# Kernel tuning notes

Hardware: AMD Instinct MI355X
Metric: run time of the kernel (lower is better)

The kernel has to match this reference:

```python
import jax, jax.numpy as jnp
import numpy as np

KH, KW, PAD = 32, 32, 10  # kernel_size and padding from NeuralMem.__init__


def setup_inputs() -> dict:
    key = jax.random.key(0)
    k1, k2, k3, k4 = jax.random.split(key, 4)
    image = jax.random.normal(k1, (64, 64, 3), dtype=jnp.float32)
    mem = jax.random.normal(k2, (8192, 3072), dtype=jnp.float32)    # faiss IndexFlatL2 bank (keys)
    mem2 = jax.random.normal(k3, (8192, 3072), dtype=jnp.float32)   # faiss reconstruction bank (values)
    mapping = jax.random.randint(k4, (8192,), 0, 8192)              # Counter.most_common(1) vote table
    return {"image": image, "mem": mem, "mem2": mem2, "mapping": mapping}


def reference(image, mem, mem2, mapping):
    H, W, C = image.shape
    x = image.transpose(2, 0, 1)                       # [C,H,W]  (permute(2,0,1))
    xp = jnp.pad(x, ((0, 0), (PAD, PAD), (PAD, PAD)))  # unfold padding
    Lh = H + 2 * PAD - KH + 1
    Lw = W + 2 * PAD - KW + 1
    ii = jnp.arange(Lh)[:, None] + jnp.arange(KH)[None, :]  # [Lh,KH]
    jj = jnp.arange(Lw)[:, None] + jnp.arange(KW)[None, :]  # [Lw,KW]
    # unfold: patches [C,Lh,KH,Lw,KW] -> [L, C*KH*KW] with torch's (C,kh,kw) column order
    patches = xp[:, ii[:, :, None, None], jj[None, None, :, :]]
    patches = patches.transpose(1, 3, 0, 2, 4).reshape(Lh * Lw, C * KH * KW)  # [L,D]
    # L2 kNN (k=1): argmin ||p - m||^2 = argmin (||m||^2 - 2 p.m); ||p||^2 is constant per row
    mem_sq = jnp.sum(mem * mem, axis=1)                # [N]
    scores = patches @ mem.T                           # [L,N]
    nn = jnp.argmin(mem_sq[None, :] - 2.0 * scores, axis=1)  # [L]
    # counter majority vote -> mem2 reconstruct
    recon = mem2[mapping[nn]]                          # [L,D]
    # fold (sum of overlapping patches), then crop padding
    rp = recon.reshape(Lh, Lw, C, KH, KW).transpose(2, 0, 3, 1, 4)  # [C,Lh,KH,Lw,KW]
    outp = jnp.zeros_like(xp).at[:, ii[:, :, None, None], jj[None, None, :, :]].add(rp)
    out = outp[:, PAD:PAD + H, PAD:PAD + W]            # [C,H,W]
    out = out / jnp.max(out)                           # out / out.flatten().max()
    return out.transpose(1, 2, 0)                      # [H,W,C]
```

## Files before the change

### kernel.cpp

```cpp
#include <hip/hip_runtime.h>

typedef unsigned short u16;
typedef unsigned int   u32;
typedef int      i32x4  __attribute__((ext_vector_type(4)));
typedef float    f32x4  __attribute__((ext_vector_type(4)));
typedef _Float16 f16x8  __attribute__((ext_vector_type(8)));

#define LHW   53
#define NP    2809
#define KDIM  3072
#define NMEM  8192
#define PADW  84
#define IMG   64
#define MPAD  2816
#define BIGF  3.402823466e+38f
#define MARGIN 24.0f
#define QS    31.75f
#define C2    (2.0f / (QS * QS))

#define O_XP    0UL
#define O_MSQ   84736UL
#define O_MI8   117504UL
#define O_AI8   25283328UL
#define O_D     33934080UL
#define O_ROWI  80071424UL
#define O_PART  80082688UL
#define O_ACC   81792256UL
#define WS_NEED3 81841408UL

#define F_XP    0
#define F_MSQ   21504
#define F_PVAL  29696
#define F_PIDX  119584
#define F_ROW   209472
#define F_ACC   212288
#define F_MAX   224576
#define NSPL    32
#define NRANGE  (NMEM / NSPL)

__device__ inline char q8(float x) {
    float y = x * QS;
    y = fminf(fmaxf(y, -127.f), 127.f);
    return (char)__float2int_rn(y);
}

__global__ void k_xp(const float* __restrict__ image, float* __restrict__ xp) {
    int id = blockIdx.x * 256 + threadIdx.x;
    if (id < 3 * PADW * PADW) {
        int c = id / (PADW * PADW), rem = id % (PADW * PADW);
        int py = rem / PADW, px = rem % PADW;
        float v = 0.f;
        if (py >= 10 && py < 74 && px >= 10 && px < 74)
            v = image[((py - 10) * IMG + (px - 10)) * 3 + c];
        xp[id] = v;
    }
}

__global__ __launch_bounds__(1024) void k_maxnorm(const float* __restrict__ acc,
                                                  float* __restrict__ out) {
    int t = threadIdx.x;
    float m = -BIGF;
    for (int i = t; i < 12288; i += 1024) m = fmaxf(m, acc[i]);
    #pragma unroll
    for (int s = 1; s < 64; s <<= 1) m = fmaxf(m, __shfl_xor(m, s));
    __shared__ float ls[16];
    int lane = t & 63, w = t >> 6;
    if (lane == 0) ls[w] = m;
    __syncthreads();
    float mv = ls[0];
    #pragma unroll
    for (int i = 1; i < 16; ++i) mv = fmaxf(mv, ls[i]);
    for (int i = t; i < 12288; i += 1024) {
        int c = i >> 12, y = (i >> 6) & 63, x = i & 63;
        out[(y * IMG + x) * 3 + c] = acc[i] / mv;
    }
}

__global__ __launch_bounds__(256) void k_quantmsq(const float* __restrict__ mem,
                                                  char* __restrict__ mq,
                                                  float* __restrict__ msq) {
    int j = blockIdx.x, t = threadIdx.x;
    const float4* r4 = (const float4*)(mem + (size_t)j * KDIM);
    char4* q4 = (char4*)(mq + (size_t)j * KDIM);
    float s = 0.f;
    #pragma unroll
    for (int i = 0; i < 3; ++i) {
        int idx = i * 256 + t;
        float4 v = r4[idx];
        s += v.x * v.x + v.y * v.y + v.z * v.z + v.w * v.w;
        char4 q = {q8(v.x), q8(v.y), q8(v.z), q8(v.w)};
        q4[idx] = q;
    }
    #pragma unroll
    for (int m = 1; m < 64; m <<= 1) s += __shfl_xor(s, m);
    __shared__ float ls[4];
    int lane = t & 63, w = t >> 6;
    if (lane == 0) ls[w] = s;
    __syncthreads();
    if (t == 0) msq[j] = ls[0] + ls[1] + ls[2] + ls[3];
}

__global__ __launch_bounds__(256) void k_quant_A(const float* __restrict__ xp,
                                                 char* __restrict__ aq) {
    int id = blockIdx.x * 256 + threadIdx.x;
    int p = id / KDIM, k = id - p * KDIM;
    float x = 0.f;
    if (p < NP) {
        int c = k >> 10, kh = (k >> 5) & 31, kw = k & 31;
        int lh = p / LHW, lw = p - lh * LHW;
        x = xp[c * (PADW * PADW) + (lh + kh) * PADW + lw + kw];
    }
    aq[id] = q8(x);
}

__global__ __launch_bounds__(256) void k_gemm_i8(
    const char* __restrict__ Aq, const char* __restrict__ Bq,
    const float* __restrict__ msq, _Float16* __restrict__ Dm)
{
    __shared__ __align__(16) char lds[32768];
    const int t = threadIdx.x;
    const int lane = t & 63;
    const int w = t >> 6, wm = w >> 1, wn = w & 1;
    const int mrow = lane & 15;

    int L = blockIdx.x;
    int logical = (L & 7) * 176 + (L >> 3);
    int by = logical / 22, bx = logical - by * 22;
    const int rowBase = bx * 128;
    const int jBase   = by * 128;

    const int q  = t >> 3;
    const int g  = t & 7;
    const int gs = g ^ (q & 7);
    const char* gp[8];
    int ldso[8];
    #pragma unroll
    for (int s = 0; s < 8; ++s) {
        int P = s >> 2, sub = s & 3;
        int row = sub * 32 + q;
        const char* basep = (P == 0 ? Aq : Bq);
        int gRow = (P == 0 ? rowBase : jBase) + row;
        gp[s]   = basep + (size_t)gRow * KDIM + g * 16;
        ldso[s] = P * 16384 + row * 128 + gs * 16;
    }

    i32x4 acc[4][4];
    #pragma unroll
    for (int i = 0; i < 4; ++i)
        #pragma unroll
        for (int j = 0; j < 4; ++j) { i32x4 z = {0, 0, 0, 0}; acc[i][j] = z; }

    i32x4 stg[8];
    #pragma unroll
    for (int s = 0; s < 8; ++s) stg[s] = *(const i32x4*)(gp[s]);

    for (int kc = 0; kc < 24; ++kc) {
        __syncthreads();
        #pragma unroll
        for (int s = 0; s < 8; ++s) *(i32x4*)(lds + ldso[s]) = stg[s];
        __syncthreads();
        if (kc < 23) {
            #pragma unroll
            for (int s = 0; s < 8; ++s)
                stg[s] = *(const i32x4*)(gp[s] + (kc + 1) * 128);
        }
        #pragma unroll
        for (int kh2 = 0; kh2 < 2; ++kh2) {
            const int grp = kh2 * 4 + (lane >> 4);
            i32x4 ah[4];
            #pragma unroll
            for (int f = 0; f < 4; ++f) {
                int ra = wm * 64 + f * 16 + mrow;
                ah[f] = *(const i32x4*)(lds + ra * 128 + (grp ^ (ra & 7)) * 16);
            }
            #pragma unroll
            for (int fj = 0; fj < 4; ++fj) {
                int rb = wn * 64 + fj * 16 + mrow;
                i32x4 bh = *(const i32x4*)(lds + 16384 + rb * 128 + (grp ^ (rb & 7)) * 16);
                #pragma unroll
                for (int fi = 0; fi < 4; ++fi)
                    acc[fi][fj] = __builtin_amdgcn_mfma_i32_16x16x64_i8(ah[fi], bh, acc[fi][fj], 0, 0, 0);
            }
        }
    }

    float ms[4];
    #pragma unroll
    for (int fj = 0; fj < 4; ++fj) ms[fj] = msq[jBase + wn * 64 + fj * 16 + mrow] - 3072.0f;
    #pragma unroll
    for (int fi = 0; fi < 4; ++fi) {
        #pragma unroll
        for (int r = 0; r < 4; ++r) {
            int p = rowBase + wm * 64 + fi * 16 + (lane >> 4) * 4 + r;
            #pragma unroll
            for (int fj = 0; fj < 4; ++fj) {
                int j = jBase + wn * 64 + fj * 16 + mrow;
                float d = fmaf(-C2, (float)acc[fi][fj][r], ms[fj]);
                Dm[(size_t)p * NMEM + j] = (_Float16)d;
            }
        }
    }
}

__global__ __launch_bounds__(256) void k_refine(
    const _Float16* __restrict__ Dm, const float* __restrict__ msq,
    const float* __restrict__ xp, const float* __restrict__ mem,
    const int* __restrict__ mapping, int* __restrict__ rowIdx)
{
    const int p = blockIdx.x, t = threadIdx.x;
    const _Float16* row = Dm + (size_t)p * NMEM;
    const int lane = t & 63, w = t >> 6;

    float bv = BIGF;
    #pragma unroll
    for (int i0 = 0; i0 < 4; ++i0) {
        f16x8 v = *(const f16x8*)(row + i0 * 2048 + t * 8);
        #pragma unroll
        for (int e = 0; e < 8; ++e) bv = fminf(bv, (float)v[e]);
    }
    #pragma unroll
    for (int m = 1; m < 64; m <<= 1) bv = fminf(bv, __shfl_xor(bv, m));
    __shared__ float wred[4];
    __shared__ int cnt;
    __shared__ int cand[128];
    if (lane == 0) wred[w] = bv;
    if (t == 0) cnt = 0;
    __syncthreads();
    float thr = fminf(fminf(wred[0], wred[1]), fminf(wred[2], wred[3])) + MARGIN;

    #pragma unroll
    for (int i0 = 0; i0 < 4; ++i0) {
        int base = i0 * 2048 + t * 8;
        f16x8 v = *(const f16x8*)(row + base);
        #pragma unroll
        for (int e = 0; e < 8; ++e)
            if ((float)v[e] <= thr) {
                int sl = atomicAdd(&cnt, 1);
                if (sl < 128) cand[sl] = base + e;
            }
    }
    __syncthreads();
    int n = min(cnt, 128);

    const int lh = p / LHW, lw = p - (p / LHW) * LHW;
    float bd = BIGF; int bj = 0x7fffffff;
    __shared__ float tot;
    for (int ci = 0; ci < n; ++ci) {
        int j = cand[ci];
        const float* mrow2 = mem + (size_t)j * KDIM;
        float s = 0.f;
        for (int k = t; k < KDIM; k += 256) {
            int c = k >> 10, kh = (k >> 5) & 31, kw = k & 31;
            s += xp[c * (PADW * PADW) + (lh + kh) * PADW + lw + kw] * mrow2[k];
        }
        #pragma unroll
        for (int m = 1; m < 64; m <<= 1) s += __shfl_xor(s, m);
        if (lane == 0) wred[w] = s;
        __syncthreads();
        if (t == 0) tot = wred[0] + wred[1] + wred[2] + wred[3];
        __syncthreads();
        float d = msq[j] - 2.f * tot;
        if (d < bd || (d == bd && j < bj)) { bd = d; bj = j; }
    }
    if (t == 0) rowIdx[p] = mapping[bj];
}

__global__ __launch_bounds__(256) void k_scatter(const float* __restrict__ mem2,
                                                 const int* __restrict__ rowIdx,
                                                 float* __restrict__ partial) {
    const int lh = blockIdx.x / 3, c = blockIdx.x % 3;
    __shared__ float accs[32 * 85];
    __shared__ int r2s[53];
    const int t = threadIdx.x;
    for (int i = t; i < 32 * 85; i += 256) accs[i] = 0.f;
    if (t < 53) r2s[t] = rowIdx[lh * LHW + t];
    __syncthreads();
    const int kh  = t >> 3;
    const int kwb = (t & 7) * 4;
    const size_t coff = (size_t)c * 1024 + kh * 32 + kwb;
    float* a0 = accs + kh * 85 + kwb;
    for (int lw = 0; lw < 53; ++lw) {
        const float4 v = *(const float4*)(mem2 + (size_t)r2s[lw] * KDIM + coff);
        float* a = a0 + lw;
        a[0] += v.x; a[1] += v.y; a[2] += v.z; a[3] += v.w;
        __syncthreads();
    }
    float* pbase = partial + ((size_t)(lh * 3 + c)) * 32 * 84;
    for (int i = t; i < 32 * 84; i += 256) {
        int kh2 = i / 84, px = i - kh2 * 84;
        pbase[i] = accs[kh2 * 85 + px];
    }
}

__global__ void k_oadd(const float* __restrict__ partial, float* __restrict__ accb) {
    int id = blockIdx.x * 256 + threadIdx.x;
    if (id >= 12288) return;
    int c = id >> 12, y = (id >> 6) & 63, x = id & 63;
    int py = y + 10, px = x + 10;
    int khmin = max(0, py - 52), khmax = min(31, py);
    float s = 0.f;
    for (int kh = khmin; kh <= khmax; ++kh) {
        int lh = py - kh;
        s += partial[((lh * 3 + c) * 32 + kh) * 84 + px];
    }
    accb[id] = s;
}

__global__ __launch_bounds__(256) void k_msq(const float* __restrict__ mem,
                                             float* __restrict__ msq) {
    int j = blockIdx.x;
    const float* row = mem + (size_t)j * KDIM;
    float s = 0.f;
    for (int i = threadIdx.x; i < KDIM; i += 256) { float v = row[i]; s += v * v; }
    #pragma unroll
    for (int m = 1; m < 64; m <<= 1) s += __shfl_xor(s, m);
    __shared__ float ls[4];
    int lane = threadIdx.x & 63, w = threadIdx.x >> 6;
    if (lane == 0) ls[w] = s;
    __syncthreads();
    if (threadIdx.x == 0) msq[j] = ls[0] + ls[1] + ls[2] + ls[3];
}

__global__ void k_amin(const float* __restrict__ pval, const int* __restrict__ pidx,
                       const int* __restrict__ mapping, int* __restrict__ rowIdx,
                       int nspl) {
    int p = blockIdx.x * 256 + threadIdx.x;
    if (p < NP) {
        float bv = BIGF; int bi = 0x7fffffff;
        for (int ns = 0; ns < nspl; ++ns) {
            float v = pval[(size_t)p * nspl + ns];
            int ix = pidx[(size_t)p * nspl + ns];
            if (v < bv || (v == bv && ix < bi)) { bv = v; bi = ix; }
        }
        rowIdx[p] = mapping[bi];
    }
}

__global__ __launch_bounds__(256) void k_gather(const float* __restrict__ mem2,
                                                const int* __restrict__ rowIdx,
                                                float* __restrict__ acc) {
    int b = blockIdx.x;
    int c = b >> 12, y = (b >> 6) & 63, x = b & 63;
    int khmin = max(0, y - 42), khmax = min(31, y + 10);
    int kwmin = max(0, x - 42), kwmax = min(31, x + 10);
    int nh = khmax - khmin + 1, nw = kwmax - kwmin + 1;
    int total = nh * nw;
    float s = 0.f;
    for (int idx = threadIdx.x; idx < total; idx += 256) {
        int kh = khmin + idx / nw;
        int kw = kwmin + idx % nw;
        int lh = y + 10 - kh, lw = x + 10 - kw;
        int p = lh * LHW + lw;
        int r2 = rowIdx[p];
        s += mem2[(size_t)r2 * KDIM + c * 1024 + kh * 32 + kw];
    }
    #pragma unroll
    for (int m = 1; m < 64; m <<= 1) s += __shfl_xor(s, m);
    __shared__ float ls[4];
    int lane = threadIdx.x & 63, w = threadIdx.x >> 6;
    if (lane == 0) ls[w] = s;
    __syncthreads();
    if (threadIdx.x == 0) acc[b] = ls[0] + ls[1] + ls[2] + ls[3];
}

__global__ __launch_bounds__(256) void k_gemm_argmin(
    const float* __restrict__ xp, const float* __restrict__ mem,
    const float* __restrict__ msq, float* __restrict__ pval,
    int* __restrict__ pidx)
{
    __shared__ float At[64][33];
    __shared__ float Bt[64][33];
    const int t = threadIdx.x;
    const int tx = t & 15, ty = t >> 4;
    const int rowBase = blockIdx.x * 64;
    const int nBase = blockIdx.y * NRANGE;

    float best[4]; int bidx[4];
    #pragma unroll
    for (int i = 0; i < 4; ++i) { best[i] = BIGF; bidx[i] = 0x7fffffff; }

    for (int nt = 0; nt < NRANGE / 64; ++nt) {
        const int jBase = nBase + nt * 64;
        float acc[4][4];
        #pragma unroll
        for (int i = 0; i < 4; ++i)
            #pragma unroll
            for (int j = 0; j < 4; ++j) acc[i][j] = 0.f;

        for (int kc = 0; kc < KDIM / 32; ++kc) {
            const int c = kc >> 5, kh = kc & 31;
            const float* xpc = xp + c * (PADW * PADW) + kh * PADW;
            #pragma unroll
            for (int i = 0; i < 8; ++i) {
                int e = i * 256 + t;
                int r = e >> 5, kwi = e & 31;
                int p = rowBase + r;
                float v = 0.f;
                if (p < NP) {
                    int lh = p / LHW, lw = p - lh * LHW;
                    v = xpc[lh * PADW + lw + kwi];
                }
                At[r][kwi] = v;
            }
            const float* mb = mem + (size_t)jBase * KDIM + kc * 32;
            #pragma unroll
            for (int i = 0; i < 8; ++i) {
                int e = i * 256 + t;
                int r = e >> 5, kwi = e & 31;
                Bt[r][kwi] = mb[(size_t)r * KDIM + kwi];
            }
            __syncthreads();
            #pragma unroll
            for (int kk = 0; kk < 32; ++kk) {
                float a[4], b[4];
                #pragma unroll
                for (int i = 0; i < 4; ++i) a[i] = At[ty + 16 * i][kk];
                #pragma unroll
                for (int j = 0; j < 4; ++j) b[j] = Bt[tx + 16 * j][kk];
                #pragma unroll
                for (int i = 0; i < 4; ++i)
                    #pragma unroll
                    for (int j = 0; j < 4; ++j) acc[i][j] += a[i] * b[j];
            }
            __syncthreads();
        }
        #pragma unroll
        for (int j = 0; j < 4; ++j) {
            int col = jBase + tx + 16 * j;
            float msv = msq[col];
            #pragma unroll
            for (int i = 0; i < 4; ++i) {
                float d = msv - 2.f * acc[i][j];
                if (d < best[i] || (d == best[i] && col < bidx[i])) {
                    best[i] = d; bidx[i] = col;
                }
            }
        }
    }
    #pragma unroll
    for (int m = 1; m < 16; m <<= 1) {
        #pragma unroll
        for (int i = 0; i < 4; ++i) {
            float ov = __shfl_xor(best[i], m);
            int   oi = __shfl_xor(bidx[i], m);
            if (ov < best[i] || (ov == best[i] && oi < bidx[i])) {
                best[i] = ov; bidx[i] = oi;
            }
        }
    }
    if (tx == 0) {
        #pragma unroll
        for (int i = 0; i < 4; ++i) {
            int p = rowBase + ty + 16 * i;
            if (p < NP) {
                pval[p * NSPL + blockIdx.y] = best[i];
                pidx[p * NSPL + blockIdx.y] = bidx[i];
            }
        }
    }
}

__global__ __launch_bounds__(256) void k_max(const float* __restrict__ acc,
                                             float* __restrict__ maxv) {
    float m = -BIGF;
    for (int i = threadIdx.x; i < 12288; i += 256) m = fmaxf(m, acc[i]);
    #pragma unroll
    for (int s = 1; s < 64; s <<= 1) m = fmaxf(m, __shfl_xor(m, s));
    __shared__ float ls[4];
    int lane = threadIdx.x & 63, w = threadIdx.x >> 6;
    if (lane == 0) ls[w] = m;
    __syncthreads();
    if (threadIdx.x == 0)
        maxv[0] = fmaxf(fmaxf(ls[0], ls[1]), fmaxf(ls[2], ls[3]));
}

__global__ void k_norm(const float* __restrict__ acc, const float* __restrict__ maxv,
                       float* __restrict__ out) {
    int id = blockIdx.x * 256 + threadIdx.x;
    if (id < 12288) {
        int c = id >> 12, y = (id >> 6) & 63, x = id & 63;
        out[(y * IMG + x) * 3 + c] = acc[id] / maxv[0];
    }
}

extern "C" void kernel_launch(void* const* d_in, const int* in_sizes, int n_in,
                              void* d_out, int out_size, void* d_ws, size_t ws_size,
                              hipStream_t stream) {
    const float* image   = (const float*)d_in[0];
    const float* mem     = (const float*)d_in[1];
    const float* mem2    = (const float*)d_in[2];
    const int*   mapping = (const int*)d_in[3];

    if (ws_size >= WS_NEED3) {
        char* wsB = (char*)d_ws;
        float*    xp   = (float*)(wsB + O_XP);
        float*    msq  = (float*)(wsB + O_MSQ);
        char*     mI8  = (char*)(wsB + O_MI8);
        char*     aI8  = (char*)(wsB + O_AI8);
        _Float16* Dm   = (_Float16*)(wsB + O_D);
        int*      rowI = (int*)(wsB + O_ROWI);
        float*    part = (float*)(wsB + O_PART);
        float*    accb = (float*)(wsB + O_ACC);

        k_xp<<<dim3((3 * PADW * PADW + 255) / 256), 256, 0, stream>>>(image, xp);
        k_quantmsq<<<dim3(NMEM), 256, 0, stream>>>(mem, mI8, msq);
        k_quant_A<<<dim3(MPAD * KDIM / 256), 256, 0, stream>>>(xp, aI8);
        k_gemm_i8<<<dim3(1408), 256, 0, stream>>>(aI8, mI8, msq, Dm);
        k_refine<<<dim3(NP), 256, 0, stream>>>(Dm, msq, xp, mem, mapping, rowI);
        k_scatter<<<dim3(LHW * 3), 256, 0, stream>>>(mem2, rowI, part);
        k_oadd<<<dim3(48), 256, 0, stream>>>(part, accb);
        k_maxnorm<<<dim3(1), 1024, 0, stream>>>(accb, (float*)d_out);
    } else {
        float* ws   = (float*)d_ws;
        float* xp   = ws + F_XP;
        float* msq  = ws + F_MSQ;
        float* pval = ws + F_PVAL;
        int*   pidx = (int*)(ws + F_PIDX);
        int*   rowI = (int*)(ws + F_ROW);
        float* acc  = ws + F_ACC;
        float* maxv = ws + F_MAX;

        k_xp<<<dim3((3 * PADW * PADW + 255) / 256), 256, 0, stream>>>(image, xp);
        k_msq<<<dim3(NMEM), 256, 0, stream>>>(mem, msq);
        k_gemm_argmin<<<dim3((NP + 63) / 64, NSPL), 256, 0, stream>>>(xp, mem, msq, pval, pidx);
        k_amin<<<dim3((NP + 255) / 256), 256, 0, stream>>>(pval, pidx, mapping, rowI, NSPL);
        k_gather<<<dim3(3 * IMG * IMG), 256, 0, stream>>>(mem2, rowI, acc);
        k_max<<<dim3(1), 256, 0, stream>>>(acc, maxv);
        k_norm<<<dim3((12288 + 255) / 256), 256, 0, stream>>>(acc, maxv, (float*)d_out);
    }
}
```

Baseline: 216.0 us.

## Double-buffer int8 GEMM with direct global-to-LDS loads and fuse row-min into epilogue

```diff
diff --git a/kernel.cpp b/kernel.cpp
--- a/kernel.cpp
+++ b/kernel.cpp
@@ -23,10 +23,12 @@
 #define O_MI8   117504UL
 #define O_AI8   25283328UL
 #define O_D     33934080UL
-#define O_ROWI  80071424UL
-#define O_PART  80082688UL
-#define O_ACC   81792256UL
-#define WS_NEED3 81841408UL
+#define O_PVAL  80071424UL
+#define O_THR   81513216UL
+#define O_ROWI  81524480UL
+#define O_PART  81535744UL
+#define O_ACC   83245312UL
+#define WS_NEED3 83294464UL
 
 #define F_XP    0
 #define F_MSQ   21504
@@ -103,21 +105,24 @@
 __global__ __launch_bounds__(256) void k_quant_A(const float* __restrict__ xp,
                                                  char* __restrict__ aq) {
     int id = blockIdx.x * 256 + threadIdx.x;
-    int p = id / KDIM, k = id - p * KDIM;
-    float x = 0.f;
+    int e0 = id * 4;
+    int p = e0 / KDIM, k = e0 - p * KDIM;
+    char4 q = {0, 0, 0, 0};
     if (p < NP) {
         int c = k >> 10, kh = (k >> 5) & 31, kw = k & 31;
         int lh = p / LHW, lw = p - lh * LHW;
-        x = xp[c * (PADW * PADW) + (lh + kh) * PADW + lw + kw];
-    }
-    aq[id] = q8(x);
+        const float* src = xp + c * (PADW * PADW) + (lh + kh) * PADW + lw + kw;
+        q.x = q8(src[0]); q.y = q8(src[1]); q.z = q8(src[2]); q.w = q8(src[3]);
+    }
+    ((char4*)aq)[id] = q;
 }
 
 __global__ __launch_bounds__(256) void k_gemm_i8(
     const char* __restrict__ Aq, const char* __restrict__ Bq,
-    const float* __restrict__ msq, _Float16* __restrict__ Dm)
+    const float* __restrict__ msq, _Float16* __restrict__ Dm,
+    float* __restrict__ pval)
 {
-    __shared__ __align__(16) char lds[32768];
+    __shared__ __align__(16) char lds[65536];
     const int t = threadIdx.x;
     const int lane = t & 63;
     const int w = t >> 6, wm = w >> 1, wn = w & 1;
@@ -129,19 +134,18 @@
     const int rowBase = bx * 128;
     const int jBase   = by * 128;
 
-    const int q  = t >> 3;
-    const int g  = t & 7;
-    const int gs = g ^ (q & 7);
-    const char* gp[8];
-    int ldso[8];
+    const int lrow = lane >> 3;
+    const int gsrc = (lane & 7) ^ lrow;
+    const char* gpl[8];
+    unsigned ldsb[8];
     #pragma unroll
     for (int s = 0; s < 8; ++s) {
         int P = s >> 2, sub = s & 3;
-        int row = sub * 32 + q;
+        int row = sub * 32 + w * 8 + lrow;
         const char* basep = (P == 0 ? Aq : Bq);
         int gRow = (P == 0 ? rowBase : jBase) + row;
-        gp[s]   = basep + (size_t)gRow * KDIM + g * 16;
-        ldso[s] = P * 16384 + row * 128 + gs * 16;
+        gpl[s]  = basep + (size_t)gRow * KDIM + gsrc * 16;
+        ldsb[s] = P * 16384 + (unsigned)(sub * 32 + w * 8) * 128;
     }
 
     i32x4 acc[4][4];
@@ -150,20 +154,26 @@
         #pragma unroll
         for (int j = 0; j < 4; ++j) { i32x4 z = {0, 0, 0, 0}; acc[i][j] = z; }
 
-    i32x4 stg[8];
-    #pragma unroll
-    for (int s = 0; s < 8; ++s) stg[s] = *(const i32x4*)(gp[s]);
+    #pragma unroll
+    for (int s = 0; s < 8; ++s)
+        __builtin_amdgcn_global_load_lds(
+            (const __attribute__((address_space(1))) void*)(gpl[s]),
+            (__attribute__((address_space(3))) void*)(lds + ldsb[s]),
+            16, 0, 0);
 
     for (int kc = 0; kc < 24; ++kc) {
-        __syncthreads();
-        #pragma unroll
-        for (int s = 0; s < 8; ++s) *(i32x4*)(lds + ldso[s]) = stg[s];
+        const int cb = kc & 1;
         __syncthreads();
         if (kc < 23) {
+            const unsigned nb = (cb ^ 1) * 32768u;
             #pragma unroll
             for (int s = 0; s < 8; ++s)
-                stg[s] = *(const i32x4*)(gp[s] + (kc + 1) * 128);
-        }
+                __builtin_amdgcn_global_load_lds(
+                    (const __attribute__((address_space(1))) void*)(gpl[s] + (kc + 1) * 128),
+                    (__attribute__((address_space(3))) void*)(lds + nb + ldsb[s]),
+                    16, 0, 0);
+        }
+        const char* lbase = lds + cb * 32768;
         #pragma unroll
         for (int kh2 = 0; kh2 < 2; ++kh2) {
             const int grp = kh2 * 4 + (lane >> 4);
@@ -171,12 +181,12 @@
             #pragma unroll
             for (int f = 0; f < 4; ++f) {
                 int ra = wm * 64 + f * 16 + mrow;
-                ah[f] = *(const i32x4*)(lds + ra * 128 + (grp ^ (ra & 7)) * 16);
+                ah[f] = *(const i32x4*)(lbase + ra * 128 + (grp ^ (ra & 7)) * 16);
             }
             #pragma unroll
             for (int fj = 0; fj < 4; ++fj) {
                 int rb = wn * 64 + fj * 16 + mrow;
-                i32x4 bh = *(const i32x4*)(lds + 16384 + rb * 128 + (grp ^ (rb & 7)) * 16);
+                i32x4 bh = *(const i32x4*)(lbase + 16384 + rb * 128 + (grp ^ (rb & 7)) * 16);
                 #pragma unroll
                 for (int fi = 0; fi < 4; ++fi)
                     acc[fi][fj] = __builtin_amdgcn_mfma_i32_16x16x64_i8(ah[fi], bh, acc[fi][fj], 0, 0, 0);
@@ -187,46 +197,58 @@
     float ms[4];
     #pragma unroll
     for (int fj = 0; fj < 4; ++fj) ms[fj] = msq[jBase + wn * 64 + fj * 16 + mrow] - 3072.0f;
+    const int splitId = by * 2 + wn;
     #pragma unroll
     for (int fi = 0; fi < 4; ++fi) {
         #pragma unroll
         for (int r = 0; r < 4; ++r) {
             int p = rowBase + wm * 64 + fi * 16 + (lane >> 4) * 4 + r;
+            float bv = BIGF;
             #pragma unroll
             for (int fj = 0; fj < 4; ++fj) {
                 int j = jBase + wn * 64 + fj * 16 + mrow;
                 float d = fmaf(-C2, (float)acc[fi][fj][r], ms[fj]);
                 Dm[(size_t)p * NMEM + j] = (_Float16)d;
-            }
-        }
+                bv = fminf(bv, d);
+            }
+            #pragma unroll
+            for (int m = 1; m < 16; m <<= 1) bv = fminf(bv, __shfl_xor(bv, m));
+            if (mrow == 0 && p < NP)
+                pval[(size_t)p * 128 + splitId] = bv;
+        }
+    }
+}
+
+__global__ void k_thr(const float* __restrict__ pval, float* __restrict__ thr) {
+    int p = blockIdx.x * 256 + threadIdx.x;
+    if (p < NP) {
+        const float4* v4 = (const float4*)(pval + (size_t)p * 128);
+        float m = BIGF;
+        #pragma unroll
+        for (int i = 0; i < 32; ++i) {
+            float4 v = v4[i];
+            m = fminf(m, fminf(fminf(v.x, v.y), fminf(v.z, v.w)));
+        }
+        thr[p] = m + (MARGIN + 0.5f);
     }
 }
 
 __global__ __launch_bounds__(256) void k_refine(
-    const _Float16* __restrict__ Dm, const float* __restrict__ msq,
-    const float* __restrict__ xp, const float* __restrict__ mem,
-    const int* __restrict__ mapping, int* __restrict__ rowIdx)
+    const _Float16* __restrict__ Dm, const float* __restrict__ thrv,
+    const float* __restrict__ msq, const float* __restrict__ xp,
+    const float* __restrict__ mem, const int* __restrict__ mapping,
+    int* __restrict__ rowIdx)
 {
     const int p = blockIdx.x, t = threadIdx.x;
     const _Float16* row = Dm + (size_t)p * NMEM;
     const int lane = t & 63, w = t >> 6;
 
-    float bv = BIGF;
-    #pragma unroll
-    for (int i0 = 0; i0 < 4; ++i0) {
-        f16x8 v = *(const f16x8*)(row + i0 * 2048 + t * 8);
-        #pragma unroll
-        for (int e = 0; e < 8; ++e) bv = fminf(bv, (float)v[e]);
-    }
-    #pragma unroll
-    for (int m = 1; m < 64; m <<= 1) bv = fminf(bv, __shfl_xor(bv, m));
     __shared__ float wred[4];
     __shared__ int cnt;
     __shared__ int cand[128];
-    if (lane == 0) wred[w] = bv;
     if (t == 0) cnt = 0;
     __syncthreads();
-    float thr = fminf(fminf(wred[0], wred[1]), fminf(wred[2], wred[3])) + MARGIN;
+    const float th = thrv[p];
 
     #pragma unroll
     for (int i0 = 0; i0 < 4; ++i0) {
@@ -234,7 +256,7 @@
         f16x8 v = *(const f16x8*)(row + base);
         #pragma unroll
         for (int e = 0; e < 8; ++e)
-            if ((float)v[e] <= thr) {
+            if ((float)v[e] <= th) {
                 int sl = atomicAdd(&cnt, 1);
                 if (sl < 128) cand[sl] = base + e;
             }
@@ -498,15 +520,18 @@
         char*     mI8  = (char*)(wsB + O_MI8);
         char*     aI8  = (char*)(wsB + O_AI8);
         _Float16* Dm   = (_Float16*)(wsB + O_D);
+        float*    pval = (float*)(wsB + O_PVAL);
+        float*    thr  = (float*)(wsB + O_THR);
         int*      rowI = (int*)(wsB + O_ROWI);
         float*    part = (float*)(wsB + O_PART);
         float*    accb = (float*)(wsB + O_ACC);
 
         k_xp<<<dim3((3 * PADW * PADW + 255) / 256), 256, 0, stream>>>(image, xp);
         k_quantmsq<<<dim3(NMEM), 256, 0, stream>>>(mem, mI8, msq);
-        k_quant_A<<<dim3(MPAD * KDIM / 256), 256, 0, stream>>>(xp, aI8);
-        k_gemm_i8<<<dim3(1408), 256, 0, stream>>>(aI8, mI8, msq, Dm);
-        k_refine<<<dim3(NP), 256, 0, stream>>>(Dm, msq, xp, mem, mapping, rowI);
+        k_quant_A<<<dim3(MPAD * KDIM / 4 / 256), 256, 0, stream>>>(xp, aI8);
+        k_gemm_i8<<<dim3(1408), 256, 0, stream>>>(aI8, mI8, msq, Dm, pval);
+        k_thr<<<dim3((NP + 255) / 256), 256, 0, stream>>>(pval, thr);
+        k_refine<<<dim3(NP), 256, 0, stream>>>(Dm, thr, msq, xp, mem, mapping, rowI);
         k_scatter<<<dim3(LHW * 3), 256, 0, stream>>>(mem2, rowI, part);
         k_oadd<<<dim3(48), 256, 0, stream>>>(part, accb);
         k_maxnorm<<<dim3(1), 1024, 0, stream>>>(accb, (float*)d_out);
```

Result: no change. 213.6 us (-1.1%).
